# Kernel tuning notes

Hardware: AMD Instinct MI355X
Metric: run time of the kernel (lower is better)

Reference implementation:

```python
import jax, jax.numpy as jnp
import numpy as np

N_NODES = 500_000
N_EDGES = 8_000_000


def setup_inputs() -> dict:
    key = jax.random.key(0)
    ks = jax.random.split(key, 10)
    x = jax.random.normal(ks[0], (N_NODES, 34), dtype=jnp.float32)
    edge_index = jax.random.randint(ks[1], (2, N_EDGES), 0, N_NODES, dtype=jnp.int32)

    def w(k, fan_in, fan_out):
        s = 1.0 / np.sqrt(fan_in)
        return jax.random.uniform(k, (fan_in, fan_out), jnp.float32, -s, s)

    return {
        "x": x,
        "edge_index": edge_index,
        "W1": w(ks[2], 34, 4), "b1": jnp.zeros((4,), jnp.float32),
        "W2": w(ks[3], 4, 4),  "b2": jnp.zeros((4,), jnp.float32),
        "W3": w(ks[4], 4, 2),  "b3": jnp.zeros((2,), jnp.float32),
        "Wl": w(ks[5], 2, 4),  "bl": jax.random.uniform(ks[6], (4,), jnp.float32, -0.7, 0.7),
    }


def reference(x, edge_index, W1, b1, W2, b2, W3, b3, Wl, bl):
    n = x.shape[0]
    # GCNConv: add self loops, symmetric normalization D^-1/2 (A+I) D^-1/2
    loops = jnp.arange(n, dtype=edge_index.dtype)
    src = jnp.concatenate([edge_index[0], loops])  # [E+N]
    dst = jnp.concatenate([edge_index[1], loops])  # [E+N]
    deg = jax.ops.segment_sum(jnp.ones_like(dst, jnp.float32), dst, num_segments=n)
    dinv = jnp.where(deg > 0, jax.lax.rsqrt(deg), 0.0)  # deg >= 1 with self loops
    norm = (dinv[src] * dinv[dst])[:, None]  # [E+N, 1]

    def gcn(h, W, b):
        h = h @ W                                   # [N, F_out] transform first
        msg = h[src] * norm                         # gather + scale per edge
        return jax.ops.segment_sum(msg, dst, num_segments=n) + b

    h = jax.nn.relu(gcn(x, W1, b1))
    h = jax.nn.relu(gcn(h, W2, b2))
    h = jax.nn.relu(gcn(h, W3, b3))   # [N, 2] -- returned as second output
    out = h @ Wl + bl                 # [N, 4]; original's out.relu() is not in-place, so no relu
    return out, h
```

## Files before the change

### kernel.cpp

```cpp
#include <hip/hip_runtime.h>
#include <hip/hip_fp16.h>
#include <hip/hip_cooperative_groups.h>

namespace cg = cooperative_groups;


#define MAXBUK 1024
#define BUCKET_BITS 9
#define BUCKET 512
#define PAD 16
#define REGION 9216

#define BIN_BLK 512
#define BIN_CHUNK 16384

#define SB_BLK 512
#define STAGE_MAX REGION

#define AGG_BLK 256
#define SMAX_A 4864

typedef unsigned u32;
typedef int      v4i __attribute__((ext_vector_type(4)));
typedef unsigned v4u __attribute__((ext_vector_type(4)));
typedef float    v2f __attribute__((ext_vector_type(2)));
typedef float    v4f __attribute__((ext_vector_type(4)));

__device__ __forceinline__ u32 ntl_u32(const u32* p) { return __builtin_nontemporal_load(p); }
__device__ __forceinline__ v4i ntl_v4i(const v4i* p) { return __builtin_nontemporal_load(p); }
__device__ __forceinline__ v4u ntl_v4u(const v4u* p) { return __builtin_nontemporal_load(p); }
__device__ __forceinline__ v4f ntl_v4f(const v4f* p) { return __builtin_nontemporal_load(p); }

__device__ __forceinline__ void unp4(uint2 pk, float& x0, float& x1, float& x2, float& x3) {
    __half2 lo = *(__half2*)&pk.x;
    __half2 hi = *(__half2*)&pk.y;
    float2 a = __half22float2(lo);
    float2 c = __half22float2(hi);
    x0 = a.x; x1 = a.y; x2 = c.x; x3 = c.y;
}

__global__ void init_kernel(int* __restrict__ gcur, int nbuk) {
    int i = blockIdx.x * 256 + threadIdx.x;
    if (i < nbuk) gcur[i * PAD] = i * REGION;
}

__global__ void __launch_bounds__(BIN_BLK, 1)
bin_kernel(const int* __restrict__ src, const int* __restrict__ dst,
           int* __restrict__ gcur, unsigned* __restrict__ ep, int E, int nbuk) {
    __shared__ int hist[MAXBUK];
    __shared__ int lbase[MAXBUK + 1];
    __shared__ int gb[MAXBUK];
    __shared__ int wsum2[8];
    __shared__ int scarry;
    __shared__ unsigned stage[BIN_CHUNK];
    int t = threadIdx.x;
    for (int b = t; b < nbuk; b += BIN_BLK) hist[b] = 0;
    if (t == 0) scarry = 0;
    __syncthreads();
    int e0 = blockIdx.x * BIN_CHUNK;
    int e1 = min(e0 + BIN_CHUNK, E);
    int cn = e1 - e0;
    const v4i* dv = (const v4i*)(dst + e0);
    const v4i* sv = (const v4i*)(src + e0);
    int n4 = cn >> 2;
    for (int i = t; i < n4; i += BIN_BLK) {
        v4i d = dv[i];
        atomicAdd(&hist[d.x >> BUCKET_BITS], 1);
        atomicAdd(&hist[d.y >> BUCKET_BITS], 1);
        atomicAdd(&hist[d.z >> BUCKET_BITS], 1);
        atomicAdd(&hist[d.w >> BUCKET_BITS], 1);
    }
    for (int e = (n4 << 2) + t; e < cn; e += BIN_BLK)
        atomicAdd(&hist[dst[e0 + e] >> BUCKET_BITS], 1);
    __syncthreads();
    for (int base = 0; base < nbuk; base += BIN_BLK) {
        int i = base + t;
        int v = (i < nbuk) ? hist[i] : 0;
        int sv2 = v;
#pragma unroll
        for (int off = 1; off < 64; off <<= 1) {
            int n = __shfl_up(sv2, off);
            if ((t & 63) >= off) sv2 += n;
        }
        if ((t & 63) == 63) wsum2[t >> 6] = sv2;
        __syncthreads();
        if (t == 0) {
            int run = scarry;
#pragma unroll
            for (int w2 = 0; w2 < 8; ++w2) { int c = wsum2[w2]; wsum2[w2] = run; run += c; }
            scarry = run;
        }
        __syncthreads();
        if (i < nbuk) lbase[i] = sv2 - v + wsum2[t >> 6];
        __syncthreads();
    }
    if (t == 0) lbase[nbuk] = scarry;
    for (int b = t; b < nbuk; b += BIN_BLK) {
        int c = hist[b];
        gb[b] = c ? atomicAdd(&gcur[b * PAD], c) : 0;
        hist[b] = 0;
    }
    __syncthreads();
    for (int i = t; i < n4; i += BIN_BLK) {
        v4i d = ntl_v4i(dv + i);
        v4i s = ntl_v4i(sv + i);
        int bk, r;
        bk = d.x >> BUCKET_BITS; r = atomicAdd(&hist[bk], 1);
        stage[lbase[bk] + r] = ((unsigned)(d.x & (BUCKET - 1)) << 23) | (unsigned)s.x;
        bk = d.y >> BUCKET_BITS; r = atomicAdd(&hist[bk], 1);
        stage[lbase[bk] + r] = ((unsigned)(d.y & (BUCKET - 1)) << 23) | (unsigned)s.y;
        bk = d.z >> BUCKET_BITS; r = atomicAdd(&hist[bk], 1);
        stage[lbase[bk] + r] = ((unsigned)(d.z & (BUCKET - 1)) << 23) | (unsigned)s.z;
        bk = d.w >> BUCKET_BITS; r = atomicAdd(&hist[bk], 1);
        stage[lbase[bk] + r] = ((unsigned)(d.w & (BUCKET - 1)) << 23) | (unsigned)s.w;
    }
    for (int e = (n4 << 2) + t; e < cn; e += BIN_BLK) {
        int d = dst[e0 + e];
        int bk = d >> BUCKET_BITS;
        int r = atomicAdd(&hist[bk], 1);
        stage[lbase[bk] + r] = ((unsigned)(d & (BUCKET - 1)) << 23) | (unsigned)src[e0 + e];
    }
    __syncthreads();
    int wid = t >> 6, lane = t & 63;
    for (int b = wid; b < nbuk; b += (BIN_BLK >> 6)) {
        int lo = lbase[b];
        int c = lbase[b + 1] - lo;
        unsigned* dp = ep + gb[b];
        for (int j = lane; j < c; j += 64)
            __builtin_nontemporal_store(stage[lo + j], dp + j);
    }
}

__global__ void __launch_bounds__(SB_BLK)
sortb_kernel(unsigned* __restrict__ ep, const int* __restrict__ gcur,
             const float* __restrict__ x, const float* __restrict__ W1,
             float* __restrict__ dinv, int* __restrict__ nodeoff,
             int* __restrict__ bend, uint2* __restrict__ g1h, int N, int nbuk) {
    __shared__ __align__(16) unsigned stage[STAGE_MAX];
    __shared__ int cnt[BUCKET];
    __shared__ int wsum[8];
    __shared__ float sW[136];
    int t = threadIdx.x, b = blockIdx.x;
    if (t < 136) sW[t] = W1[t];
    cnt[t] = 0;
    int ps = b * REGION;
    int cn = min(gcur[b * PAD] - ps, STAGE_MAX);
    const v4u* epv = (const v4u*)(ep + ps);
    int n4 = cn >> 2;
    for (int j = t; j < n4; j += SB_BLK) ((v4u*)stage)[j] = ntl_v4u(epv + j);
    for (int j = (n4 << 2) + t; j < cn; j += SB_BLK) stage[j] = ntl_u32(ep + ps + j);
    if (t == 0) bend[b] = ps + cn;
    __syncthreads();
    for (int j = t; j < cn; j += SB_BLK) atomicAdd(&cnt[stage[j] >> 23], 1);
    __syncthreads();
    int deg = cnt[t];
    float dv = rsqrtf((float)deg + 1.0f);
    int v = deg;
#pragma unroll
    for (int off = 1; off < 64; off <<= 1) {
        int n = __shfl_up(v, off);
        if ((t & 63) >= off) v += n;
    }
    if ((t & 63) == 63) wsum[t >> 6] = v;
    __syncthreads();
    if (t == 0) {
        int run = 0;
#pragma unroll
        for (int w = 0; w < 8; ++w) { int c = wsum[w]; wsum[w] = run; run += c; }
    }
    __syncthreads();
    int excl = v + wsum[t >> 6] - deg;
    int gbase = b << BUCKET_BITS;
    int nn = min(BUCKET, N - gbase);
    if (t < nn) { nodeoff[gbase + t] = ps + excl; dinv[gbase + t] = dv; }
    cnt[t] = excl;
    __syncthreads();
    for (int j = t; j < cn; j += SB_BLK) {
        unsigned u = stage[j];
        int r = atomicAdd(&cnt[u >> 23], 1);
        ep[ps + r] = u & 0x7FFFFFu;
    }
    __syncthreads();
    ((float*)cnt)[t] = dv;
    float* xs = (float*)stage;
    for (int hh = 0; hh < 2; ++hh) {
        int rl = hh << 8;
        int rows = nn - rl; rows = rows < 0 ? 0 : (rows > 256 ? 256 : rows);
        if (rows > 0) {
            if (hh == 1) __syncthreads();
            int nfl = rows * 34;
            const float* xsrc = x + (size_t)(gbase + rl) * 34;
            int n4f = nfl >> 2;
            for (int j = t; j < n4f; j += SB_BLK)
                ((v4f*)xs)[j] = ntl_v4f((const v4f*)xsrc + j);
            for (int j = (n4f << 2) + t; j < nfl; j += SB_BLK) xs[j] = xsrc[j];
            __syncthreads();
            if (t < rows) {
                float dvv = ((float*)cnt)[rl + t];
                const float* xr = xs + t * 34;
                float o0 = 0.f, o1 = 0.f, o2 = 0.f, o3 = 0.f;
#pragma unroll
                for (int k = 0; k < 17; ++k) {
                    float vx = xr[2 * k], vy = xr[2 * k + 1];
                    o0 = fmaf(vx, sW[(2 * k) * 4 + 0], o0);
                    o1 = fmaf(vx, sW[(2 * k) * 4 + 1], o1);
                    o2 = fmaf(vx, sW[(2 * k) * 4 + 2], o2);
                    o3 = fmaf(vx, sW[(2 * k) * 4 + 3], o3);
                    o0 = fmaf(vy, sW[(2 * k + 1) * 4 + 0], o0);
                    o1 = fmaf(vy, sW[(2 * k + 1) * 4 + 1], o1);
                    o2 = fmaf(vy, sW[(2 * k + 1) * 4 + 2], o2);
                    o3 = fmaf(vy, sW[(2 * k + 1) * 4 + 3], o3);
                }
                __half2 lo = __floats2half2_rn(o0 * dvv, o1 * dvv);
                __half2 hi = __floats2half2_rn(o2 * dvv, o3 * dvv);
                uint2 pk;
                pk.x = *(unsigned*)&lo;
                pk.y = *(unsigned*)&hi;
                g1h[gbase + rl + t] = pk;
            }
        }
    }
}

#define ACC4(Q) { float t0,t1,t2,t3; unp4(Q,t0,t1,t2,t3); a0+=t0; a1+=t1; a2+=t2; a3+=t3; }

__device__ __forceinline__ void phase1(int i, int lo, int hi, int cs, int s,
        const unsigned* se, const unsigned* __restrict__ esrc,
        const uint2* __restrict__ g1h, float dv,
        const float* __restrict__ b1, const float* __restrict__ W2,
        uint2* __restrict__ g2h) {
    float a0, a1, a2, a3;
    unp4(g1h[i], a0, a1, a2, a3);
    int hi2 = min(hi, cs);
    int j = lo;
    for (; j + 8 <= hi2; j += 8) {
        unsigned s0 = se[j], s1 = se[j+1], s2 = se[j+2], s3 = se[j+3];
        unsigned s4 = se[j+4], s5 = se[j+5], s6 = se[j+6], s7 = se[j+7];
        uint2 q0 = g1h[s0], q1 = g1h[s1], q2 = g1h[s2], q3 = g1h[s3];
        uint2 q4 = g1h[s4], q5 = g1h[s5], q6 = g1h[s6], q7 = g1h[s7];
        ACC4(q0) ACC4(q1) ACC4(q2) ACC4(q3) ACC4(q4) ACC4(q5) ACC4(q6) ACC4(q7)
    }
    for (; j + 4 <= hi2; j += 4) {
        unsigned s0 = se[j], s1 = se[j+1], s2 = se[j+2], s3 = se[j+3];
        uint2 q0 = g1h[s0], q1 = g1h[s1], q2 = g1h[s2], q3 = g1h[s3];
        ACC4(q0) ACC4(q1) ACC4(q2) ACC4(q3)
    }
    for (; j < hi2; ++j) ACC4(g1h[se[j]])
    for (; j < hi; ++j) ACC4(g1h[ntl_u32(esrc + s + j)])
    float h0 = fmaxf(fmaf(a0, dv, b1[0]), 0.f);
    float h1 = fmaxf(fmaf(a1, dv, b1[1]), 0.f);
    float h2 = fmaxf(fmaf(a2, dv, b1[2]), 0.f);
    float h3 = fmaxf(fmaf(a3, dv, b1[3]), 0.f);
    float o0 = dv * (h0 * W2[0] + h1 * W2[4] + h2 * W2[8] + h3 * W2[12]);
    float o1 = dv * (h0 * W2[1] + h1 * W2[5] + h2 * W2[9] + h3 * W2[13]);
    float o2 = dv * (h0 * W2[2] + h1 * W2[6] + h2 * W2[10] + h3 * W2[14]);
    float o3 = dv * (h0 * W2[3] + h1 * W2[7] + h2 * W2[11] + h3 * W2[15]);
    __half2 lo2 = __floats2half2_rn(o0, o1);
    __half2 hi3 = __floats2half2_rn(o2, o3);
    uint2 pk;
    pk.x = *(unsigned*)&lo2;
    pk.y = *(unsigned*)&hi3;
    g2h[i] = pk;
}

__device__ __forceinline__ void phase2(int i, int lo, int hi, int cs, int s,
        const unsigned* se, const unsigned* __restrict__ esrc,
        const uint2* __restrict__ g2h, float dv,
        const float* __restrict__ b2, const float* __restrict__ W3,
        unsigned* __restrict__ g3h) {
    float a0, a1, a2, a3;
    unp4(g2h[i], a0, a1, a2, a3);
    int hi2 = min(hi, cs);
    int j = lo;
    for (; j + 8 <= hi2; j += 8) {
        unsigned s0 = se[j], s1 = se[j+1], s2 = se[j+2], s3 = se[j+3];
        unsigned s4 = se[j+4], s5 = se[j+5], s6 = se[j+6], s7 = se[j+7];
        uint2 q0 = g2h[s0], q1 = g2h[s1], q2 = g2h[s2], q3 = g2h[s3];
        uint2 q4 = g2h[s4], q5 = g2h[s5], q6 = g2h[s6], q7 = g2h[s7];
        ACC4(q0) ACC4(q1) ACC4(q2) ACC4(q3) ACC4(q4) ACC4(q5) ACC4(q6) ACC4(q7)
    }
    for (; j + 4 <= hi2; j += 4) {
        unsigned s0 = se[j], s1 = se[j+1], s2 = se[j+2], s3 = se[j+3];
        uint2 q0 = g2h[s0], q1 = g2h[s1], q2 = g2h[s2], q3 = g2h[s3];
        ACC4(q0) ACC4(q1) ACC4(q2) ACC4(q3)
    }
    for (; j < hi2; ++j) ACC4(g2h[se[j]])
    for (; j < hi; ++j) ACC4(g2h[ntl_u32(esrc + s + j)])
    float h0 = fmaxf(fmaf(a0, dv, b2[0]), 0.f);
    float h1 = fmaxf(fmaf(a1, dv, b2[1]), 0.f);
    float h2 = fmaxf(fmaf(a2, dv, b2[2]), 0.f);
    float h3 = fmaxf(fmaf(a3, dv, b2[3]), 0.f);
    float o0 = dv * (h0 * W3[0] + h1 * W3[2] + h2 * W3[4] + h3 * W3[6]);
    float o1 = dv * (h0 * W3[1] + h1 * W3[3] + h2 * W3[5] + h3 * W3[7]);
    __half2 oo = __floats2half2_rn(o0, o1);
    g3h[i] = *(unsigned*)&oo;
}

__device__ __forceinline__ void phase3(int i, int lo, int hi, int cs, int s,
        const unsigned* se, const unsigned* __restrict__ esrc,
        const unsigned* __restrict__ g3h, float dv,
        const float* __restrict__ b3, const float* __restrict__ Wl,
        const float* __restrict__ bl, float* __restrict__ out, int N) {
    unsigned pk = g3h[i];
    float2 v = __half22float2(*(__half2*)&pk);
    float ax = v.x, ay = v.y;
    int hi2 = min(hi, cs);
    int j = lo;
    for (; j + 8 <= hi2; j += 8) {
        unsigned q0 = g3h[se[j]],   q1 = g3h[se[j+1]], q2 = g3h[se[j+2]], q3 = g3h[se[j+3]];
        unsigned q4 = g3h[se[j+4]], q5 = g3h[se[j+5]], q6 = g3h[se[j+6]], q7 = g3h[se[j+7]];
        float2 v0 = __half22float2(*(__half2*)&q0);
        float2 v1 = __half22float2(*(__half2*)&q1);
        float2 v2 = __half22float2(*(__half2*)&q2);
        float2 v3 = __half22float2(*(__half2*)&q3);
        float2 v4 = __half22float2(*(__half2*)&q4);
        float2 v5 = __half22float2(*(__half2*)&q5);
        float2 v6 = __half22float2(*(__half2*)&q6);
        float2 v7 = __half22float2(*(__half2*)&q7);
        ax += (v0.x + v1.x + v2.x + v3.x) + (v4.x + v5.x + v6.x + v7.x);
        ay += (v0.y + v1.y + v2.y + v3.y) + (v4.y + v5.y + v6.y + v7.y);
    }
    for (; j + 4 <= hi2; j += 4) {
        unsigned q0 = g3h[se[j]], q1 = g3h[se[j+1]], q2 = g3h[se[j+2]], q3 = g3h[se[j+3]];
        float2 v0 = __half22float2(*(__half2*)&q0);
        float2 v1 = __half22float2(*(__half2*)&q1);
        float2 v2 = __half22float2(*(__half2*)&q2);
        float2 v3 = __half22float2(*(__half2*)&q3);
        ax += v0.x + v1.x + v2.x + v3.x;
        ay += v0.y + v1.y + v2.y + v3.y;
    }
    for (; j < hi2; ++j) {
        unsigned q = g3h[se[j]];
        float2 w = __half22float2(*(__half2*)&q);
        ax += w.x; ay += w.y;
    }
    for (; j < hi; ++j) {
        unsigned q = g3h[ntl_u32(esrc + s + j)];
        float2 w = __half22float2(*(__half2*)&q);
        ax += w.x; ay += w.y;
    }
    float h0 = fmaxf(fmaf(ax, dv, b3[0]), 0.f);
    float h1 = fmaxf(fmaf(ay, dv, b3[1]), 0.f);
    v4f oo;
    oo.x = fmaf(h0, Wl[0], fmaf(h1, Wl[4], bl[0]));
    oo.y = fmaf(h0, Wl[1], fmaf(h1, Wl[5], bl[1]));
    oo.z = fmaf(h0, Wl[2], fmaf(h1, Wl[6], bl[2]));
    oo.w = fmaf(h0, Wl[3], fmaf(h1, Wl[7], bl[3]));
    __builtin_nontemporal_store(oo, (v4f*)out + i);
    v2f h; h.x = h0; h.y = h1;
    __builtin_nontemporal_store(h, (v2f*)(out + (size_t)4 * N) + i);
}

struct BlkGeo { int s, cs, lo, hi; bool act; int i; float dv; };

__device__ __forceinline__ BlkGeo geo(const int* __restrict__ nodeoff,
                                      const int* __restrict__ bend,
                                      const float* __restrict__ dinv, int N) {
    BlkGeo g;
    int t = threadIdx.x, blk = blockIdx.x, buk = blk >> 1;
    int gbase = (buk << BUCKET_BITS) + ((blk & 1) << 8);
    int nn = min(256, N - gbase);
    g.i = gbase + t;
    g.act = (nn > 0) && (t < nn);
    g.s = 0; g.cs = 0; g.lo = 0; g.hi = 0; g.dv = 0.f;
    if (nn > 0) {
        g.s = nodeoff[gbase];
        int nbn = min(512, N - (buk << BUCKET_BITS));
        bool lasthalf = (blk & 1) ? true : (nbn <= 256);
        int e = lasthalf ? bend[buk] : nodeoff[gbase + 256];
        g.cs = min(e - g.s, SMAX_A);
        if (g.act) {
            bool lastnode = lasthalf && (t == nn - 1);
            g.lo = nodeoff[g.i] - g.s;
            g.hi = (lastnode ? bend[buk] : nodeoff[g.i + 1]) - g.s;
            g.dv = dinv[g.i];
        }
    }
    return g;
}

__global__ void __launch_bounds__(AGG_BLK, 8)
aggf_kernel(const unsigned* __restrict__ esrc, const int* __restrict__ nodeoff,
            const int* __restrict__ bend, const float* __restrict__ dinv,
            uint2* __restrict__ g1h, uint2* __restrict__ g2h,
            const float* __restrict__ b1, const float* __restrict__ W2,
            const float* __restrict__ b2, const float* __restrict__ W3,
            const float* __restrict__ b3, const float* __restrict__ Wl,
            const float* __restrict__ bl, float* __restrict__ out, int N) {
    cg::grid_group gg = cg::this_grid();
    __shared__ unsigned se[SMAX_A];
    BlkGeo g = geo(nodeoff, bend, dinv, N);
    int t = threadIdx.x;
    for (int j = t; j < g.cs; j += AGG_BLK) se[j] = ntl_u32(esrc + g.s + j);
    __syncthreads();
    if (g.act) phase1(g.i, g.lo, g.hi, g.cs, g.s, se, esrc, g1h, g.dv, b1, W2, g2h);
    gg.sync();
    unsigned* g3h = (unsigned*)g1h;
    if (g.act) phase2(g.i, g.lo, g.hi, g.cs, g.s, se, esrc, g2h, g.dv, b2, W3, g3h);
    gg.sync();
    if (g.act) phase3(g.i, g.lo, g.hi, g.cs, g.s, se, esrc, g3h, g.dv, b3, Wl, bl, out, N);
}

template <int P>
__global__ void __launch_bounds__(AGG_BLK)
aggp_kernel(const unsigned* __restrict__ esrc, const int* __restrict__ nodeoff,
            const int* __restrict__ bend, const float* __restrict__ dinv,
            uint2* __restrict__ g1h, uint2* __restrict__ g2h,
            const float* __restrict__ b1, const float* __restrict__ W2,
            const float* __restrict__ b2, const float* __restrict__ W3,
            const float* __restrict__ b3, const float* __restrict__ Wl,
            const float* __restrict__ bl, float* __restrict__ out, int N) {
    __shared__ unsigned se[SMAX_A];
    BlkGeo g = geo(nodeoff, bend, dinv, N);
    int t = threadIdx.x;
    for (int j = t; j < g.cs; j += AGG_BLK) se[j] = ntl_u32(esrc + g.s + j);
    __syncthreads();
    unsigned* g3h = (unsigned*)g1h;
    if (g.act) {
        if (P == 1) phase1(g.i, g.lo, g.hi, g.cs, g.s, se, esrc, g1h, g.dv, b1, W2, g2h);
        if (P == 2) phase2(g.i, g.lo, g.hi, g.cs, g.s, se, esrc, g2h, g.dv, b2, W3, g3h);
        if (P == 3) phase3(g.i, g.lo, g.hi, g.cs, g.s, se, esrc, g3h, g.dv, b3, Wl, bl, out, N);
    }
}

extern "C" void kernel_launch(void* const* d_in, const int* in_sizes, int n_in,
                              void* d_out, int out_size, void* d_ws, size_t ws_size,
                              hipStream_t stream) {
    const float* x  = (const float*)d_in[0];
    const int*   ei = (const int*)d_in[1];
    const float* W1 = (const float*)d_in[2];
    const float* b1 = (const float*)d_in[3];
    const float* W2 = (const float*)d_in[4];
    const float* b2 = (const float*)d_in[5];
    const float* W3 = (const float*)d_in[6];
    const float* b3 = (const float*)d_in[7];
    const float* Wl = (const float*)d_in[8];
    const float* bl = (const float*)d_in[9];
    float* out = (float*)d_out;

    int N = in_sizes[0] / 34;
    const int E = in_sizes[1] / 2;
    const int* src = ei;
    const int* dst = ei + E;
    const int NBUK = (N + BUCKET - 1) >> BUCKET_BITS;

    auto al16 = [](size_t v) { return (v + 15) & ~(size_t)15; };
    char* w = (char*)d_ws;
    size_t off = 0;
    int*      gcur    = (int*)(w + off);      off += al16((size_t)NBUK * PAD * 4);
    int*      bend    = (int*)(w + off);      off += al16((size_t)NBUK * 4);
    float*    dinv    = (float*)(w + off);    off += al16((size_t)N * 4);
    int*      nodeoff = (int*)(w + off);      off += al16((size_t)(N + 1) * 4);
    unsigned* ep      = (unsigned*)(w + off); off += al16((size_t)NBUK * REGION * 4);
    uint2*    g1h     = (uint2*)(w + off);    off += al16((size_t)(N + 1) * 8);
    uint2*    g2h     = (uint2*)(w + off);

    const int nb_bin = (E + BIN_CHUNK - 1) / BIN_CHUNK;
    const int nb_agg = 2 * NBUK;

    init_kernel<<<(NBUK + 255) / 256, 256, 0, stream>>>(gcur, NBUK);
    bin_kernel<<<nb_bin, BIN_BLK, 0, stream>>>(src, dst, gcur, ep, E, NBUK);
    sortb_kernel<<<NBUK, SB_BLK, 0, stream>>>(ep, gcur, x, W1, dinv, nodeoff, bend, g1h, N, NBUK);

    int blocksPerCU = 0, ncu = 0, dev = 0;
    hipGetDevice(&dev);
    hipDeviceGetAttribute(&ncu, hipDeviceAttributeMultiprocessorCount, dev);
    hipOccupancyMaxActiveBlocksPerMultiprocessor(&blocksPerCU, (const void*)aggf_kernel, AGG_BLK, 0);
    if (blocksPerCU * ncu >= nb_agg) {
        void* args[] = {(void*)&ep, (void*)&nodeoff, (void*)&bend, (void*)&dinv,
                        (void*)&g1h, (void*)&g2h, (void*)&b1, (void*)&W2,
                        (void*)&b2, (void*)&W3, (void*)&b3, (void*)&Wl,
                        (void*)&bl, (void*)&out, (void*)&N};
        hipLaunchCooperativeKernel((const void*)aggf_kernel, dim3(nb_agg), dim3(AGG_BLK),
                                   args, 0, stream);
    } else {
        aggp_kernel<1><<<nb_agg, AGG_BLK, 0, stream>>>(ep, nodeoff, bend, dinv, g1h, g2h,
                                                       b1, W2, b2, W3, b3, Wl, bl, out, N);
        aggp_kernel<2><<<nb_agg, AGG_BLK, 0, stream>>>(ep, nodeoff, bend, dinv, g1h, g2h,
                                                       b1, W2, b2, W3, b3, Wl, bl, out, N);
        aggp_kernel<3><<<nb_agg, AGG_BLK, 0, stream>>>(ep, nodeoff, bend, dinv, g1h, g2h,
                                                       b1, W2, b2, W3, b3, Wl, bl, out, N);
    }
}
```

Before: 266.3 us.

## Cache packed dst buckets in LDS, fuse degree count into load, vectorize edge staging

The binning kernel now reads dst only once, keeping bucket and offset packed in shared memory for the scatter pass. This costs an extra LDS array, so the chunk size is halved to keep per-block LDS roughly the same. The sort kernel counts degrees while loading the staged edges instead of in a separate pass over LDS. The aggregation kernels stage edge sources with aligned 16-byte loads instead of scalar loads. Smaller chunks double the number of bin blocks and their global atomic reservations per bucket.

Result: slower. 288.0 us (+8.2%).

```diff
diff --git a/kernel.cpp b/kernel.cpp
--- a/kernel.cpp
+++ b/kernel.cpp
@@ -12,7 +12,7 @@
 #define REGION 9216
 
 #define BIN_BLK 512
-#define BIN_CHUNK 16384
+#define BIN_CHUNK 8192
 
 #define SB_BLK 512
 #define STAGE_MAX REGION
@@ -52,6 +52,7 @@
     __shared__ int gb[MAXBUK];
     __shared__ int wsum2[8];
     __shared__ int scarry;
+    __shared__ unsigned dpk[BIN_CHUNK];
     __shared__ unsigned stage[BIN_CHUNK];
     int t = threadIdx.x;
     for (int b = t; b < nbuk; b += BIN_BLK) hist[b] = 0;
@@ -61,17 +62,27 @@
     int e1 = min(e0 + BIN_CHUNK, E);
     int cn = e1 - e0;
     const v4i* dv = (const v4i*)(dst + e0);
-    const v4i* sv = (const v4i*)(src + e0);
     int n4 = cn >> 2;
     for (int i = t; i < n4; i += BIN_BLK) {
-        v4i d = dv[i];
-        atomicAdd(&hist[d.x >> BUCKET_BITS], 1);
-        atomicAdd(&hist[d.y >> BUCKET_BITS], 1);
-        atomicAdd(&hist[d.z >> BUCKET_BITS], 1);
-        atomicAdd(&hist[d.w >> BUCKET_BITS], 1);
-    }
-    for (int e = (n4 << 2) + t; e < cn; e += BIN_BLK)
-        atomicAdd(&hist[dst[e0 + e] >> BUCKET_BITS], 1);
+        v4i d = ntl_v4i(dv + i);
+        int b0 = d.x >> BUCKET_BITS, b1_ = d.y >> BUCKET_BITS;
+        int b2_ = d.z >> BUCKET_BITS, b3_ = d.w >> BUCKET_BITS;
+        atomicAdd(&hist[b0], 1);
+        atomicAdd(&hist[b1_], 1);
+        atomicAdd(&hist[b2_], 1);
+        atomicAdd(&hist[b3_], 1);
+        int p = 4 * i;
+        dpk[p + 0] = ((unsigned)b0 << BUCKET_BITS) | (unsigned)(d.x & (BUCKET - 1));
+        dpk[p + 1] = ((unsigned)b1_ << BUCKET_BITS) | (unsigned)(d.y & (BUCKET - 1));
+        dpk[p + 2] = ((unsigned)b2_ << BUCKET_BITS) | (unsigned)(d.z & (BUCKET - 1));
+        dpk[p + 3] = ((unsigned)b3_ << BUCKET_BITS) | (unsigned)(d.w & (BUCKET - 1));
+    }
+    for (int e = (n4 << 2) + t; e < cn; e += BIN_BLK) {
+        int d = dst[e0 + e];
+        int bk = d >> BUCKET_BITS;
+        atomicAdd(&hist[bk], 1);
+        dpk[e] = ((unsigned)bk << BUCKET_BITS) | (unsigned)(d & (BUCKET - 1));
+    }
     __syncthreads();
     for (int base = 0; base < nbuk; base += BIN_BLK) {
         int i = base + t;
@@ -101,24 +112,26 @@
         hist[b] = 0;
     }
     __syncthreads();
+    const v4i* sv = (const v4i*)(src + e0);
     for (int i = t; i < n4; i += BIN_BLK) {
-        v4i d = ntl_v4i(dv + i);
         v4i s = ntl_v4i(sv + i);
-        int bk, r;
-        bk = d.x >> BUCKET_BITS; r = atomicAdd(&hist[bk], 1);
-        stage[lbase[bk] + r] = ((unsigned)(d.x & (BUCKET - 1)) << 23) | (unsigned)s.x;
-        bk = d.y >> BUCKET_BITS; r = atomicAdd(&hist[bk], 1);
-        stage[lbase[bk] + r] = ((unsigned)(d.y & (BUCKET - 1)) << 23) | (unsigned)s.y;
-        bk = d.z >> BUCKET_BITS; r = atomicAdd(&hist[bk], 1);
-        stage[lbase[bk] + r] = ((unsigned)(d.z & (BUCKET - 1)) << 23) | (unsigned)s.z;
-        bk = d.w >> BUCKET_BITS; r = atomicAdd(&hist[bk], 1);
-        stage[lbase[bk] + r] = ((unsigned)(d.w & (BUCKET - 1)) << 23) | (unsigned)s.w;
+        int p = 4 * i;
+        unsigned v0 = dpk[p], v1 = dpk[p + 1], v2 = dpk[p + 2], v3 = dpk[p + 3];
+        int bk; unsigned r;
+        bk = (int)(v0 >> BUCKET_BITS); r = (unsigned)atomicAdd(&hist[bk], 1);
+        stage[lbase[bk] + r] = ((v0 & (BUCKET - 1u)) << 23) | (unsigned)s.x;
+        bk = (int)(v1 >> BUCKET_BITS); r = (unsigned)atomicAdd(&hist[bk], 1);
+        stage[lbase[bk] + r] = ((v1 & (BUCKET - 1u)) << 23) | (unsigned)s.y;
+        bk = (int)(v2 >> BUCKET_BITS); r = (unsigned)atomicAdd(&hist[bk], 1);
+        stage[lbase[bk] + r] = ((v2 & (BUCKET - 1u)) << 23) | (unsigned)s.z;
+        bk = (int)(v3 >> BUCKET_BITS); r = (unsigned)atomicAdd(&hist[bk], 1);
+        stage[lbase[bk] + r] = ((v3 & (BUCKET - 1u)) << 23) | (unsigned)s.w;
     }
     for (int e = (n4 << 2) + t; e < cn; e += BIN_BLK) {
-        int d = dst[e0 + e];
-        int bk = d >> BUCKET_BITS;
-        int r = atomicAdd(&hist[bk], 1);
-        stage[lbase[bk] + r] = ((unsigned)(d & (BUCKET - 1)) << 23) | (unsigned)src[e0 + e];
+        unsigned v = dpk[e];
+        int bk = (int)(v >> BUCKET_BITS);
+        unsigned r = (unsigned)atomicAdd(&hist[bk], 1);
+        stage[lbase[bk] + r] = ((v & (BUCKET - 1u)) << 23) | (unsigned)src[e0 + e];
     }
     __syncthreads();
     int wid = t >> 6, lane = t & 63;
@@ -145,13 +158,23 @@
     cnt[t] = 0;
     int ps = b * REGION;
     int cn = min(gcur[b * PAD] - ps, STAGE_MAX);
+    if (t == 0) bend[b] = ps + cn;
+    __syncthreads();
     const v4u* epv = (const v4u*)(ep + ps);
     int n4 = cn >> 2;
-    for (int j = t; j < n4; j += SB_BLK) ((v4u*)stage)[j] = ntl_v4u(epv + j);
-    for (int j = (n4 << 2) + t; j < cn; j += SB_BLK) stage[j] = ntl_u32(ep + ps + j);
-    if (t == 0) bend[b] = ps + cn;
-    __syncthreads();
-    for (int j = t; j < cn; j += SB_BLK) atomicAdd(&cnt[stage[j] >> 23], 1);
+    for (int j = t; j < n4; j += SB_BLK) {
+        v4u u = ntl_v4u(epv + j);
+        ((v4u*)stage)[j] = u;
+        atomicAdd(&cnt[u.x >> 23], 1);
+        atomicAdd(&cnt[u.y >> 23], 1);
+        atomicAdd(&cnt[u.z >> 23], 1);
+        atomicAdd(&cnt[u.w >> 23], 1);
+    }
+    for (int j = (n4 << 2) + t; j < cn; j += SB_BLK) {
+        unsigned u = ntl_u32(ep + ps + j);
+        stage[j] = u;
+        atomicAdd(&cnt[u >> 23], 1);
+    }
     __syncthreads();
     int deg = cnt[t];
     float dv = rsqrtf((float)deg + 1.0f);
@@ -379,6 +402,21 @@
     return g;
 }
 
+__device__ __forceinline__ void stage_se(unsigned* se, const unsigned* __restrict__ esrc,
+                                         int s, int cs, int t) {
+    int head = (4 - (s & 3)) & 3;
+    if (head > cs) head = cs;
+    for (int j = t; j < head; j += AGG_BLK) se[j] = ntl_u32(esrc + s + j);
+    int nv = (cs - head) >> 2;
+    const v4u* evp = (const v4u*)(esrc + s + head);
+    for (int j = t; j < nv; j += AGG_BLK) {
+        v4u u = ntl_v4u(evp + j);
+        int p = head + 4 * j;
+        se[p] = u.x; se[p + 1] = u.y; se[p + 2] = u.z; se[p + 3] = u.w;
+    }
+    for (int j = head + (nv << 2) + t; j < cs; j += AGG_BLK) se[j] = ntl_u32(esrc + s + j);
+}
+
 __global__ void __launch_bounds__(AGG_BLK, 8)
 aggf_kernel(const unsigned* __restrict__ esrc, const int* __restrict__ nodeoff,
             const int* __restrict__ bend, const float* __restrict__ dinv,
@@ -391,7 +429,7 @@
     __shared__ unsigned se[SMAX_A];
     BlkGeo g = geo(nodeoff, bend, dinv, N);
     int t = threadIdx.x;
-    for (int j = t; j < g.cs; j += AGG_BLK) se[j] = ntl_u32(esrc + g.s + j);
+    stage_se(se, esrc, g.s, g.cs, t);
     __syncthreads();
     if (g.act) phase1(g.i, g.lo, g.hi, g.cs, g.s, se, esrc, g1h, g.dv, b1, W2, g2h);
     gg.sync();
@@ -413,7 +451,7 @@
     __shared__ unsigned se[SMAX_A];
     BlkGeo g = geo(nodeoff, bend, dinv, N);
     int t = threadIdx.x;
-    for (int j = t; j < g.cs; j += AGG_BLK) se[j] = ntl_u32(esrc + g.s + j);
+    stage_se(se, esrc, g.s, g.cs, t);
     __syncthreads();
     unsigned* g3h = (unsigned*)g1h;
     if (g.act) {
```
